# Optimization experiments

Hardware: AMD Instinct MI355X
Metric: run time of the kernel (lower is better)

Reference implementation:

```python
import jax, jax.numpy as jnp
import numpy as np

N = 524288
MAXV = 8  # rect-rect intersection has at most 8 vertices
EPS = 1e-8


def setup_inputs() -> dict:
    key = jax.random.key(0)
    k1, k2, k3 = jax.random.split(key, 3)
    return {
        "box": jax.random.normal(k1, (N, 11), jnp.float32),
        "box_target": jax.random.normal(k2, (N, 11), jnp.float32),
        "weight": jax.random.uniform(k3, (N, 11), jnp.float32),
        "avg_factor": N // 2,
    }


def decode_box(box):
    # [x,y,z,logW,logL,logH,sin,cos,v...] -> [x,y,z,W,L,H,yaw,v...]
    yaw = jnp.arctan2(box[..., 6], box[..., 7])
    return jnp.concatenate(
        [box[..., :3], jnp.exp(box[..., 3:6]), yaw[..., None], box[..., 8:]], axis=-1)


def get_rect_vertices(bev):
    # bev: (5,) = [cx, cy, w, l, yaw] -> (4, 2) corners, CCW, rotated about center
    cx, cy, w, l, yaw = bev[0], bev[1], bev[2], bev[3], bev[4]
    dx, dy = w / 2, l / 2
    lx = jnp.stack([-dx, dx, dx, -dx])
    ly = jnp.stack([-dy, -dy, dy, dy])
    s, c = jnp.sin(yaw), jnp.cos(yaw)
    return jnp.stack([lx * c - ly * s + cx, lx * s + ly * c + cy], axis=-1)


def clip_halfplane(poly, count, a, b):
    # Sutherland-Hodgman clip of poly (MAXV,2) with `count` valid verts
    # against left side of directed edge a->b. Fixed-size buffer + mask.
    d = b - a  # (2,)
    idx = jnp.arange(MAXV)
    cnt = jnp.maximum(count, 1)
    prev = poly[(idx - 1) % cnt]
    cur = poly

    def is_left(p):
        return d[0] * (p[..., 1] - a[1]) - d[1] * (p[..., 0] - a[0]) >= 0

    cur_in, prev_in = is_left(cur), is_left(prev)
    num = (a[0] - prev[:, 0]) * d[1] - (a[1] - prev[:, 1]) * d[0]
    den = (cur[:, 0] - prev[:, 0]) * d[1] - (cur[:, 1] - prev[:, 1]) * d[0] + EPS
    ip = prev + (num / den)[:, None] * (cur - prev)  # edge/halfplane intersection
    valid = idx < count
    emit_ip = valid & (prev_in ^ cur_in)   # crossing edge -> emit intersection
    emit_cur = valid & cur_in              # inside vertex -> emit it
    # interleave per-input-edge outputs in original order (ip, then cur)
    pts = jnp.stack([ip, cur], axis=1).reshape(2 * MAXV, 2)
    emit = jnp.stack([emit_ip, emit_cur], axis=1).reshape(2 * MAXV)
    pos = jnp.where(emit, jnp.cumsum(emit) - 1, MAXV)  # compact valid pts to front
    out = jnp.zeros((MAXV, 2), poly.dtype).at[pos].set(
        jnp.where(emit[:, None], pts, 0.0), mode="drop")
    return out, jnp.minimum(emit.sum(), MAXV).astype(jnp.int32)


def poly_area(poly, count):
    # shoelace over the `count` valid vertices
    idx = jnp.arange(MAXV)
    nxt = poly[(idx + 1) % jnp.maximum(count, 1)]
    cross = jnp.where(idx < count, poly[:, 0] * nxt[:, 1] - poly[:, 1] * nxt[:, 0], 0.0)
    return jnp.abs(cross.sum() / 2.0)


def giou_one(bev1, bev2):
    v1 = get_rect_vertices(bev1)  # (4,2)
    v2 = get_rect_vertices(bev2)
    poly = jnp.zeros((MAXV, 2), bev1.dtype).at[:4].set(v1)
    count = jnp.int32(4)
    for i in range(4):  # clip subject rect by 4 half-planes of clip rect
        poly, count = clip_halfplane(poly, count, v2[i], v2[(i + 1) % 4])
        count = jnp.where(count < 3, 0, count)  # degenerate -> empty (original break)
    inter = poly_area(poly, count)
    area1 = bev1[2] * bev1[3]
    area2 = bev2[2] * bev2[3]
    union = area1 + area2 - inter
    allp = jnp.concatenate([v1, v2], axis=0)
    enclosing = (allp[:, 0].max() - allp[:, 0].min()) * (allp[:, 1].max() - allp[:, 1].min())
    iou = inter / (union + EPS)
    return iou - (enclosing - union) / (enclosing + EPS)


def _bev(dec):
    return jnp.stack([dec[:, 0], dec[:, 1], dec[:, 3], dec[:, 4], dec[:, 6]], axis=-1)


def reference(box, box_target, weight, avg_factor):
    af = max(float(avg_factor), 1.0)
    # L1 box loss (reg_weights are all 1.0 per init defaults)
    loss_box = (jnp.abs(box - box_target) * weight).sum() / af
    # rotated BEV GIoU loss
    bev_p = _bev(decode_box(box))
    bev_t = _bev(decode_box(box_target))
    giou = jax.vmap(giou_one)(bev_p, bev_t)
    loss_giou = (1.0 - giou).sum() / af
    return loss_box, loss_giou
```

## Files before the change

### kernel.cpp

```cpp
#include <hip/hip_runtime.h>

#define BLOCK 256
#define ITERS 2
#define EPSF 1e-8f

typedef float f4u __attribute__((ext_vector_type(4), aligned(4)));

struct Row9 { f4u b0, b1, b2, t0, t1, t2, w0, w1, w2; };

__device__ __forceinline__ Row9 load_row(const float* __restrict__ box,
                                         const float* __restrict__ tgt,
                                         const float* __restrict__ wgt,
                                         size_t r) {
    Row9 R;
    R.b0 = *(const f4u*)(box + r); R.b1 = *(const f4u*)(box + r + 4); R.b2 = *(const f4u*)(box + r + 7);
    R.t0 = *(const f4u*)(tgt + r); R.t1 = *(const f4u*)(tgt + r + 4); R.t2 = *(const f4u*)(tgt + r + 7);
    R.w0 = *(const f4u*)(wgt + r); R.w1 = *(const f4u*)(wgt + r + 4); R.w2 = *(const f4u*)(wgt + r + 7);
    return R;
}

__device__ __forceinline__ float safe_rcp(float d) {
    float sd = (fabsf(d) > 1e-30f) ? d : copysignf(1e-30f, d);
    return __frcp_rn(sd);
}

__device__ __forceinline__ float clip_len(float px, float py,
                                          float rdx, float rdy,
                                          float hx, float hy) {
    float t1x = (-hx - px) * rdx, t2x = (hx - px) * rdx;
    float t1y = (-hy - py) * rdy, t2y = (hy - py) * rdy;
    float tmin = fmaxf(fmaxf(fminf(t1x, t2x), fminf(t1y, t2y)), 0.f);
    float tmax = fminf(fminf(fmaxf(t1x, t2x), fmaxf(t1y, t2y)), 1.f);
    return fmaxf(tmax - tmin, 0.f);
}

__device__ __forceinline__ void box_compute(const Row9& R, float& l1out, float& gout)
{
    f4u b0 = R.b0, b1 = R.b1, b2 = R.b2;
    f4u t0 = R.t0, t1 = R.t1, t2 = R.t2;
    f4u w0 = R.w0, w1 = R.w1, w2 = R.w2;

    float lb = 0.f;
    lb += fabsf(b0.x - t0.x) * w0.x;
    lb += fabsf(b0.y - t0.y) * w0.y;
    lb += fabsf(b0.z - t0.z) * w0.z;
    lb += fabsf(b0.w - t0.w) * w0.w;
    lb += fabsf(b1.x - t1.x) * w1.x;
    lb += fabsf(b1.y - t1.y) * w1.y;
    lb += fabsf(b1.z - t1.z) * w1.z;
    lb += fabsf(b1.w - t1.w) * w1.w;
    lb += fabsf(b2.y - t2.y) * w2.y;
    lb += fabsf(b2.z - t2.z) * w2.z;
    lb += fabsf(b2.w - t2.w) * w2.w;
    l1out = lb;

    float cx1 = b0.x, cy1 = b0.y, cx2 = t0.x, cy2 = t0.y;
    float w1v = __expf(b0.w), l1v = __expf(b1.x);
    float w2v = __expf(t0.w), l2v = __expf(t1.x);
    float r1 = rsqrtf(fmaxf(b1.z * b1.z + b1.w * b1.w, 1e-30f));
    float s1 = b1.z * r1, c1 = b1.w * r1;
    float r2 = rsqrtf(fmaxf(t1.z * t1.z + t1.w * t1.w, 1e-30f));
    float s2 = t1.z * r2, c2 = t1.w * r2;

    float hx1 = 0.5f * w1v, hy1 = 0.5f * l1v;
    float hx2 = 0.5f * w2v, hy2 = 0.5f * l2v;

    float e1x = fabsf(hx1 * c1) + fabsf(hy1 * s1);
    float e1y = fabsf(hx1 * s1) + fabsf(hy1 * c1);
    float e2x = fabsf(hx2 * c2) + fabsf(hy2 * s2);
    float e2y = fabsf(hx2 * s2) + fabsf(hy2 * c2);
    float enc = (fmaxf(cx1 + e1x, cx2 + e2x) - fminf(cx1 - e1x, cx2 - e2x))
              * (fmaxf(cy1 + e1y, cy2 + e2y) - fminf(cy1 - e1y, cy2 - e2y));

    float dxw = cx1 - cx2, dyw = cy1 - cy2;
    float txl =  c2 * dxw + s2 * dyw;
    float tyl = -s2 * dxw + c2 * dyw;
    float cr_ = c1 * c2 + s1 * s2;
    float sr_ = s1 * c2 - c1 * s2;

    float ax_ = hx1 * cr_, ay_ = hx1 * sr_;
    float bx_ = hy1 * sr_, by_ = hy1 * cr_;
    float q0x = txl - ax_ + bx_, q0y = tyl - ay_ - by_;
    float q1x = txl + ax_ + bx_, q1y = tyl + ay_ - by_;
    float q2x = txl + ax_ - bx_, q2y = tyl + ay_ + by_;
    float q3x = txl - ax_ - bx_, q3y = tyl - ay_ + by_;

    float inter2 = 0.f;

    {
        float d01x = 2.f * ax_, d01y = 2.f * ay_;
        float d12x = -2.f * bx_, d12y = 2.f * by_;
        float r01x = safe_rcp(d01x), r01y = safe_rcp(d01y);
        float r12x = safe_rcp(d12x), r12y = safe_rcp(d12y);

        float L0 = clip_len(q0x, q0y,  r01x,  r01y, hx2, hy2);
        inter2 += L0 * (q0x * d01y - q0y * d01x);
        float L1 = clip_len(q1x, q1y,  r12x,  r12y, hx2, hy2);
        inter2 += L1 * (q1x * d12y - q1y * d12x);
        float L2 = clip_len(q2x, q2y, -r01x, -r01y, hx2, hy2);
        inter2 += L2 * (q2y * d01x - q2x * d01y);
        float L3 = clip_len(q3x, q3y, -r12x, -r12y, hx2, hy2);
        inter2 += L3 * (q3y * d12x - q3x * d12y);
    }

    {
        float zx = -hx2 - txl, zy = -hy2 - tyl;
        float u0x =  cr_ * zx + sr_ * zy;
        float u0y = -sr_ * zx + cr_ * zy;
        float E0x =  2.f * hx2 * cr_, E0y = -2.f * hx2 * sr_;
        float E1x =  2.f * hy2 * sr_, E1y =  2.f * hy2 * cr_;
        float u1x = u0x + E0x, u1y = u0y + E0y;
        float u2x = u1x + E1x, u2y = u1y + E1y;
        float u3x = u0x + E1x, u3y = u0y + E1y;
        float re0x = safe_rcp(E0x), re0y = safe_rcp(E0y);
        float re1x = safe_rcp(E1x), re1y = safe_rcp(E1y);

        float tsum = 0.f;
        tsum += clip_len(u0x, u0y,  re0x,  re0y, hx1, hy1);
        tsum += clip_len(u1x, u1y,  re1x,  re1y, hx1, hy1);
        tsum += clip_len(u2x, u2y, -re0x, -re0y, hx1, hy1);
        tsum += clip_len(u3x, u3y, -re1x, -re1y, hx1, hy1);
        inter2 += 2.f * hx2 * hy2 * tsum;
    }

    float inter = 0.5f * fabsf(inter2);
    float areaU = w1v * l1v + w2v * l2v - inter;
    float iou = inter / (areaU + EPSF);
    float giou = iou - (enc - areaU) / (enc + EPSF);
    gout = 1.f - giou;
}

__global__ __launch_bounds__(BLOCK, 4) void box_loss_main(
    const float* __restrict__ box, const float* __restrict__ tgt,
    const float* __restrict__ wgt, int n, int T, float* __restrict__ partials)
{
    __shared__ float red[8];

    const int tid = threadIdx.x;
    int i = blockIdx.x * BLOCK + tid;
    float sumL1 = 0.f, sumG = 0.f;

    bool v = i < n;
    Row9 cur = load_row(box, tgt, wgt, (size_t)(v ? i : 0) * 11);

#pragma unroll
    for (int k = 0; k < ITERS; ++k) {
        int inext = i + T;
        bool vnext = false;
        Row9 nxt;
        if (k + 1 < ITERS) {
            vnext = inext < n;
            nxt = load_row(box, tgt, wgt, (size_t)(vnext ? inext : 0) * 11);
        }
        float l1, g;
        box_compute(cur, l1, g);
        sumL1 += v ? l1 : 0.f;
        sumG  += v ? g  : 0.f;
        if (k + 1 < ITERS) { cur = nxt; v = vnext; i = inext; }
    }

#pragma unroll
    for (int off = 32; off > 0; off >>= 1) {
        sumL1 += __shfl_down(sumL1, off);
        sumG  += __shfl_down(sumG, off);
    }
    const int wave = tid >> 6, lane = tid & 63;
    if (lane == 0) { red[wave] = sumL1; red[4 + wave] = sumG; }
    __syncthreads();
    if (tid == 0) {
        partials[2 * (size_t)blockIdx.x]     = red[0] + red[1] + red[2] + red[3];
        partials[2 * (size_t)blockIdx.x + 1] = red[4] + red[5] + red[6] + red[7];
    }
}

__global__ __launch_bounds__(256) void box_loss_final(
    const float* __restrict__ partials, int nblk,
    const int* __restrict__ avg_factor, float* __restrict__ out)
{
    __shared__ float red[8];
    float a = 0.f, g = 0.f;
    for (int i = threadIdx.x; i < nblk; i += 256) {
        a += partials[2 * (size_t)i];
        g += partials[2 * (size_t)i + 1];
    }
#pragma unroll
    for (int off = 32; off > 0; off >>= 1) {
        a += __shfl_down(a, off);
        g += __shfl_down(g, off);
    }
    const int wave = threadIdx.x >> 6, lane = threadIdx.x & 63;
    if (lane == 0) { red[wave] = a; red[4 + wave] = g; }
    __syncthreads();
    if (threadIdx.x == 0) {
        float af = (float)(*avg_factor);
        if (af < 1.f) af = 1.f;
        out[0] = (red[0] + red[1] + red[2] + red[3]) / af;
        out[1] = (red[4] + red[5] + red[6] + red[7]) / af;
    }
}

extern "C" void kernel_launch(void* const* d_in, const int* in_sizes, int n_in,
                              void* d_out, int out_size, void* d_ws, size_t ws_size,
                              hipStream_t stream) {
    const float* box = (const float*)d_in[0];
    const float* tgt = (const float*)d_in[1];
    const float* wgt = (const float*)d_in[2];
    const int*   af  = (const int*)d_in[3];
    float* out = (float*)d_out;
    float* partials = (float*)d_ws;

    int n = in_sizes[0] / 11;
    int nblk = (n + BLOCK * ITERS - 1) / (BLOCK * ITERS);
    if (nblk < 1) nblk = 1;
    int T = nblk * BLOCK;

    hipLaunchKernelGGL(box_loss_main, dim3(nblk), dim3(BLOCK), 0, stream,
                       box, tgt, wgt, n, T, partials);
    hipLaunchKernelGGL(box_loss_final, dim3(1), dim3(256), 0, stream,
                       partials, nblk, af, out);
}
```

Baseline: 19.40 us.

## Load rows as coalesced float4 chunks per wave and transpose via LDS

```diff
diff --git a/kernel.cpp b/kernel.cpp
--- a/kernel.cpp
+++ b/kernel.cpp
@@ -4,19 +4,15 @@
 #define ITERS 2
 #define EPSF 1e-8f
 
-typedef float f4u __attribute__((ext_vector_type(4), aligned(4)));
-
-struct Row9 { f4u b0, b1, b2, t0, t1, t2, w0, w1, w2; };
-
-__device__ __forceinline__ Row9 load_row(const float* __restrict__ box,
-                                         const float* __restrict__ tgt,
-                                         const float* __restrict__ wgt,
-                                         size_t r) {
-    Row9 R;
-    R.b0 = *(const f4u*)(box + r); R.b1 = *(const f4u*)(box + r + 4); R.b2 = *(const f4u*)(box + r + 7);
-    R.t0 = *(const f4u*)(tgt + r); R.t1 = *(const f4u*)(tgt + r + 4); R.t2 = *(const f4u*)(tgt + r + 7);
-    R.w0 = *(const f4u*)(wgt + r); R.w1 = *(const f4u*)(wgt + r + 4); R.w2 = *(const f4u*)(wgt + r + 7);
-    return R;
+#define CHUNKS 176
+
+struct Nine { float4 b0, b1, b2, t0, t1, t2, w0, w1, w2; };
+
+__device__ __forceinline__ long lmin(long a, long b) { return a < b ? a : b; }
+
+__device__ __forceinline__ float l1c(float4 b, float4 t, float4 w) {
+    return fabsf(b.x - t.x) * w.x + fabsf(b.y - t.y) * w.y +
+           fabsf(b.z - t.z) * w.z + fabsf(b.w - t.w) * w.w;
 }
 
 __device__ __forceinline__ float safe_rcp(float d) {
@@ -34,33 +30,16 @@
     return fmaxf(tmax - tmin, 0.f);
 }
 
-__device__ __forceinline__ void box_compute(const Row9& R, float& l1out, float& gout)
+__device__ __forceinline__ float giou_term(
+    float cx1, float cy1, float lw1, float ll1, float sy1, float cw1,
+    float cx2, float cy2, float lw2, float ll2, float sy2, float cw2)
 {
-    f4u b0 = R.b0, b1 = R.b1, b2 = R.b2;
-    f4u t0 = R.t0, t1 = R.t1, t2 = R.t2;
-    f4u w0 = R.w0, w1 = R.w1, w2 = R.w2;
-
-    float lb = 0.f;
-    lb += fabsf(b0.x - t0.x) * w0.x;
-    lb += fabsf(b0.y - t0.y) * w0.y;
-    lb += fabsf(b0.z - t0.z) * w0.z;
-    lb += fabsf(b0.w - t0.w) * w0.w;
-    lb += fabsf(b1.x - t1.x) * w1.x;
-    lb += fabsf(b1.y - t1.y) * w1.y;
-    lb += fabsf(b1.z - t1.z) * w1.z;
-    lb += fabsf(b1.w - t1.w) * w1.w;
-    lb += fabsf(b2.y - t2.y) * w2.y;
-    lb += fabsf(b2.z - t2.z) * w2.z;
-    lb += fabsf(b2.w - t2.w) * w2.w;
-    l1out = lb;
-
-    float cx1 = b0.x, cy1 = b0.y, cx2 = t0.x, cy2 = t0.y;
-    float w1v = __expf(b0.w), l1v = __expf(b1.x);
-    float w2v = __expf(t0.w), l2v = __expf(t1.x);
-    float r1 = rsqrtf(fmaxf(b1.z * b1.z + b1.w * b1.w, 1e-30f));
-    float s1 = b1.z * r1, c1 = b1.w * r1;
-    float r2 = rsqrtf(fmaxf(t1.z * t1.z + t1.w * t1.w, 1e-30f));
-    float s2 = t1.z * r2, c2 = t1.w * r2;
+    float w1v = __expf(lw1), l1v = __expf(ll1);
+    float w2v = __expf(lw2), l2v = __expf(ll2);
+    float r1 = rsqrtf(fmaxf(sy1 * sy1 + cw1 * cw1, 1e-30f));
+    float s1 = sy1 * r1, c1 = cw1 * r1;
+    float r2 = rsqrtf(fmaxf(sy2 * sy2 + cw2 * cw2, 1e-30f));
+    float s2 = sy2 * r2, c2 = cw2 * r2;
 
     float hx1 = 0.5f * w1v, hy1 = 0.5f * l1v;
     float hx2 = 0.5f * w2v, hy2 = 0.5f * l2v;
@@ -86,13 +65,11 @@
     float q3x = txl - ax_ - bx_, q3y = tyl - ay_ + by_;
 
     float inter2 = 0.f;
-
     {
         float d01x = 2.f * ax_, d01y = 2.f * ay_;
         float d12x = -2.f * bx_, d12y = 2.f * by_;
         float r01x = safe_rcp(d01x), r01y = safe_rcp(d01y);
         float r12x = safe_rcp(d12x), r12y = safe_rcp(d12y);
-
         float L0 = clip_len(q0x, q0y,  r01x,  r01y, hx2, hy2);
         inter2 += L0 * (q0x * d01y - q0y * d01x);
         float L1 = clip_len(q1x, q1y,  r12x,  r12y, hx2, hy2);
@@ -102,7 +79,6 @@
         float L3 = clip_len(q3x, q3y, -r12x, -r12y, hx2, hy2);
         inter2 += L3 * (q3y * d12x - q3x * d12y);
     }
-
     {
         float zx = -hx2 - txl, zy = -hy2 - tyl;
         float u0x =  cr_ * zx + sr_ * zy;
@@ -114,7 +90,6 @@
         float u3x = u0x + E1x, u3y = u0y + E1y;
         float re0x = safe_rcp(E0x), re0y = safe_rcp(E0y);
         float re1x = safe_rcp(E1x), re1y = safe_rcp(E1y);
-
         float tsum = 0.f;
         tsum += clip_len(u0x, u0y,  re0x,  re0y, hx1, hy1);
         tsum += clip_len(u1x, u1y,  re1x,  re1y, hx1, hy1);
@@ -127,36 +102,69 @@
     float areaU = w1v * l1v + w2v * l2v - inter;
     float iou = inter / (areaU + EPSF);
     float giou = iou - (enc - areaU) / (enc + EPSF);
-    gout = 1.f - giou;
-}
-
-__global__ __launch_bounds__(BLOCK, 4) void box_loss_main(
-    const float* __restrict__ box, const float* __restrict__ tgt,
-    const float* __restrict__ wgt, int n, int T, float* __restrict__ partials)
+    return 1.f - giou;
+}
+
+__global__ __launch_bounds__(BLOCK) void box_loss_main(
+    const float4* __restrict__ b4, const float4* __restrict__ t4,
+    const float4* __restrict__ w4, int n, float* __restrict__ partials)
 {
+    __shared__ float4 lds[4][2][CHUNKS];
     __shared__ float red[8];
 
-    const int tid = threadIdx.x;
-    int i = blockIdx.x * BLOCK + tid;
+    const int tid = threadIdx.x, wv = tid >> 6, lane = tid & 63;
+    const long nf  = (long)n * 11;
+    const long ncl = (nf >> 2) > 0 ? (nf >> 2) : 1;
+    const bool third = lane < 48;
+
     float sumL1 = 0.f, sumG = 0.f;
 
-    bool v = i < n;
-    Row9 cur = load_row(box, tgt, wgt, (size_t)(v ? i : 0) * 11);
+    const long base = (long)blockIdx.x * (BLOCK * ITERS) + wv * 64;
+
+    Nine cur, nxt;
+    {
+        long cb = (base * 11) >> 2;
+        long i0 = lmin(cb + lane, ncl - 1);
+        long i1 = lmin(cb + lane + 64, ncl - 1);
+        long i2 = lmin(cb + (third ? lane : 47) + 128, ncl - 1);
+        cur.b0 = b4[i0]; cur.b1 = b4[i1]; cur.b2 = b4[i2];
+        cur.t0 = t4[i0]; cur.t1 = t4[i1]; cur.t2 = t4[i2];
+        cur.w0 = w4[i0]; cur.w1 = w4[i1]; cur.w2 = w4[i2];
+    }
 
 #pragma unroll
     for (int k = 0; k < ITERS; ++k) {
-        int inext = i + T;
-        bool vnext = false;
-        Row9 nxt;
+        const long wb = base + (long)k * BLOCK;
         if (k + 1 < ITERS) {
-            vnext = inext < n;
-            nxt = load_row(box, tgt, wgt, (size_t)(vnext ? inext : 0) * 11);
+            long cb = ((wb + BLOCK) * 11) >> 2;
+            long i0 = lmin(cb + lane, ncl - 1);
+            long i1 = lmin(cb + lane + 64, ncl - 1);
+            long i2 = lmin(cb + (third ? lane : 47) + 128, ncl - 1);
+            nxt.b0 = b4[i0]; nxt.b1 = b4[i1]; nxt.b2 = b4[i2];
+            nxt.t0 = t4[i0]; nxt.t1 = t4[i1]; nxt.t2 = t4[i2];
+            nxt.w0 = w4[i0]; nxt.w1 = w4[i1]; nxt.w2 = w4[i2];
         }
-        float l1, g;
-        box_compute(cur, l1, g);
-        sumL1 += v ? l1 : 0.f;
-        sumG  += v ? g  : 0.f;
-        if (k + 1 < ITERS) { cur = nxt; v = vnext; i = inext; }
+
+        const long cb = (wb * 11) >> 2;
+        if (cb + lane < ncl)               sumL1 += l1c(cur.b0, cur.t0, cur.w0);
+        if (cb + lane + 64 < ncl)          sumL1 += l1c(cur.b1, cur.t1, cur.w1);
+        if (third && cb + lane + 128 < ncl) sumL1 += l1c(cur.b2, cur.t2, cur.w2);
+
+        lds[wv][0][lane] = cur.b0; lds[wv][0][lane + 64] = cur.b1;
+        if (third) lds[wv][0][lane + 128] = cur.b2;
+        lds[wv][1][lane] = cur.t0; lds[wv][1][lane + 64] = cur.t1;
+        if (third) lds[wv][1][lane + 128] = cur.t2;
+
+        asm volatile("s_waitcnt lgkmcnt(0)" ::: "memory");
+        __builtin_amdgcn_sched_barrier(0);
+
+        const float* rb = (const float*)&lds[wv][0][0] + lane * 11;
+        const float* rt = (const float*)&lds[wv][1][0] + lane * 11;
+        float g = giou_term(rb[0], rb[1], rb[3], rb[4], rb[6], rb[7],
+                            rt[0], rt[1], rt[3], rt[4], rt[6], rt[7]);
+        sumG += ((wb + lane) < n) ? g : 0.f;
+
+        if (k + 1 < ITERS) cur = nxt;
     }
 
 #pragma unroll
@@ -164,8 +172,7 @@
         sumL1 += __shfl_down(sumL1, off);
         sumG  += __shfl_down(sumG, off);
     }
-    const int wave = tid >> 6, lane = tid & 63;
-    if (lane == 0) { red[wave] = sumL1; red[4 + wave] = sumG; }
+    if (lane == 0) { red[wv] = sumL1; red[4 + wv] = sumG; }
     __syncthreads();
     if (tid == 0) {
         partials[2 * (size_t)blockIdx.x]     = red[0] + red[1] + red[2] + red[3];
@@ -202,20 +209,19 @@
 extern "C" void kernel_launch(void* const* d_in, const int* in_sizes, int n_in,
                               void* d_out, int out_size, void* d_ws, size_t ws_size,
                               hipStream_t stream) {
-    const float* box = (const float*)d_in[0];
-    const float* tgt = (const float*)d_in[1];
-    const float* wgt = (const float*)d_in[2];
-    const int*   af  = (const int*)d_in[3];
+    const float4* b4 = (const float4*)d_in[0];
+    const float4* t4 = (const float4*)d_in[1];
+    const float4* w4 = (const float4*)d_in[2];
+    const int*    af = (const int*)d_in[3];
     float* out = (float*)d_out;
     float* partials = (float*)d_ws;
 
     int n = in_sizes[0] / 11;
     int nblk = (n + BLOCK * ITERS - 1) / (BLOCK * ITERS);
     if (nblk < 1) nblk = 1;
-    int T = nblk * BLOCK;
 
     hipLaunchKernelGGL(box_loss_main, dim3(nblk), dim3(BLOCK), 0, stream,
-                       box, tgt, wgt, n, T, partials);
+                       b4, t4, w4, n, partials);
     hipLaunchKernelGGL(box_loss_final, dim3(1), dim3(256), 0, stream,
                        partials, nblk, af, out);
 }
```

Result: slower. 21.13 us (+8.9%).
